# Kernel optimization log

Measured on AMD Instinct MI355X. Metric: run time of the kernel, lower is better.

The kernel has to match this reference:

```python
import jax, jax.numpy as jnp
import numpy as np

B, H, S, D = 1, 32, 2048, 128
LAST_Q = 64      # MInference uses the last 64 queries to estimate the pattern
V_TOPK = 256     # top vertical columns kept per head
S_TOPK = 512     # top slash diagonals kept per head
N_SINK = 4       # vertical columns always kept (attention sink)
N_LOCAL = 64     # local diagonals always kept
SCALE = 1.0 / np.sqrt(D)


def setup_inputs() -> dict:
    key = jax.random.key(0)
    k1, k2, k3 = jax.random.split(key, 3)
    q = jax.random.normal(k1, (B, H, S, D), jnp.float32)
    k = jax.random.normal(k2, (B, H, S, D), jnp.float32)
    v = jax.random.normal(k3, (B, H, S, D), jnp.float32)
    return {"q": q, "k": k, "v": v}


def _vertical_slash_masks(q, k):
    """Estimate per-head vertical/slash importance from the last LAST_Q queries
    and return boolean column mask [B,H,S] and diagonal mask [B,H,S]."""
    ql = q[:, :, -LAST_Q:, :]                                   # [B,H,LQ,D]
    est = jnp.einsum('bhqd,bhkd->bhqk', ql, k) * SCALE          # [B,H,LQ,S]
    rows = jnp.arange(S - LAST_Q, S)                            # global row ids
    cols = jnp.arange(S)
    causal = rows[:, None] >= cols[None, :]                     # [LQ,S]
    est = jnp.where(causal, est, -jnp.inf)
    p = jax.nn.softmax(est, axis=-1)                            # [B,H,LQ,S]

    # vertical importance: column sums of estimated attention
    vertical = p.sum(axis=2)                                    # [B,H,S]

    # slash importance: sums along diagonals d = row - col (d in [0, S-1])
    diag = jnp.clip(rows[:, None] - cols[None, :], 0, S - 1)    # negatives are causally masked (p=0)
    flat_d = diag.reshape(-1)
    flat_p = p.reshape(B * H, LAST_Q * S)
    slash = jax.vmap(lambda pr: jax.ops.segment_sum(pr, flat_d, num_segments=S))(flat_p)
    slash = slash.reshape(B, H, S)                              # [B,H,S]

    # always keep sink columns and the local diagonal band
    vertical = vertical.at[..., :N_SINK].set(jnp.inf)
    slash = slash.at[..., :N_LOCAL].set(jnp.inf)

    _, v_idx = jax.lax.top_k(vertical, V_TOPK)                  # [B,H,V_TOPK]
    _, s_idx = jax.lax.top_k(slash, S_TOPK)                     # [B,H,S_TOPK]

    scatter_true = jax.vmap(jax.vmap(lambda m, i: m.at[i].set(True)))
    vmask = scatter_true(jnp.zeros((B, H, S), bool), v_idx)     # which columns kept
    smask = scatter_true(jnp.zeros((B, H, S), bool), s_idx)     # which diagonals kept
    return vmask, smask


def reference(q, k, v):
    vmask, smask = _vertical_slash_masks(q, k)

    rows = jnp.arange(S)
    cols = jnp.arange(S)
    causal = rows[:, None] >= cols[None, :]                     # [S,S]
    d = jnp.clip(rows[:, None] - cols[None, :], 0, S - 1)       # [S,S] diagonal id

    # keep (r,c) if causal AND (column c is a top vertical OR diagonal r-c is a top slash)
    keep = causal[None, None] & (vmask[:, :, None, :] | jnp.take(smask, d, axis=-1))

    scores = jnp.einsum('bhqd,bhkd->bhqk', q, k) * SCALE        # [B,H,S,S]
    scores = jnp.where(keep, scores, -jnp.inf)
    probs = jax.nn.softmax(scores, axis=-1)                     # every row keeps diagonal 0 -> no all-masked rows
    return jnp.einsum('bhqk,bhkd->bhqd', probs, v)
```

## Files before the change

### kernel.cpp

```cpp
#include <hip/hip_runtime.h>
#include <hip/hip_bf16.h>

#define S_LEN 2048
#define NH 32
#define D_DIM 128
#define LAST_Q 64
#define SCALE_F 0.08838834764831845f
#define QSCALE (0.08838834764831845f * 1.4426950408889634f)
#define RESCALE_THR 11.54f

typedef __attribute__((ext_vector_type(8))) short bf16x8;
typedef __attribute__((ext_vector_type(4))) float f32x4;
typedef unsigned long long u64;
typedef unsigned int u32;
typedef unsigned short u16;

static __device__ __forceinline__ u16 f32_bf16(float f) {
  u32 u = __float_as_uint(f);
  u32 r = (u + 0x7FFFu + ((u >> 16) & 1u)) >> 16;
  return (u16)r;
}

static __device__ __forceinline__ u32 cvt_pk_bf16(float lo, float hi) {
  u32 r;
  asm("v_cvt_pk_bf16_f32 %0, %1, %2" : "=v"(r) : "v"(lo), "v"(hi));
  return r;
}

__global__ __launch_bounds__(256) void conv_kernel(const float* __restrict__ k,
                                                   const float* __restrict__ v,
                                                   u16* __restrict__ kpre,
                                                   u16* __restrict__ vpre) {
  int bid = blockIdx.x;
  int t = bid & 31, h = bid >> 5;
  int tid = threadIdx.x;
  int c0 = t * 64;
  __shared__ u16 Vb[64][136];
  for (int i = tid; i < 512; i += 256) {
    int r = i >> 3, s = i & 7;
    const float* srcp = v + ((size_t)(h * S_LEN + c0 + r)) * D_DIM + s * 16;
    float4 f0 = *(const float4*)(srcp);
    float4 f1 = *(const float4*)(srcp + 4);
    float4 f2 = *(const float4*)(srcp + 8);
    float4 f3 = *(const float4*)(srcp + 12);
    bf16x8 t0, t1;
    t0[0] = (short)f32_bf16(f0.x); t0[1] = (short)f32_bf16(f0.y);
    t0[2] = (short)f32_bf16(f0.z); t0[3] = (short)f32_bf16(f0.w);
    t0[4] = (short)f32_bf16(f1.x); t0[5] = (short)f32_bf16(f1.y);
    t0[6] = (short)f32_bf16(f1.z); t0[7] = (short)f32_bf16(f1.w);
    t1[0] = (short)f32_bf16(f2.x); t1[1] = (short)f32_bf16(f2.y);
    t1[2] = (short)f32_bf16(f2.z); t1[3] = (short)f32_bf16(f2.w);
    t1[4] = (short)f32_bf16(f3.x); t1[5] = (short)f32_bf16(f3.y);
    t1[6] = (short)f32_bf16(f3.z); t1[7] = (short)f32_bf16(f3.w);
    *(bf16x8*)&Vb[r][s * 16] = t0;
    *(bf16x8*)&Vb[r][s * 16 + 8] = t1;
  }
  u16* kp = kpre + (size_t)h * 262144 + (size_t)t * 8192;
#pragma unroll
  for (int j = 0; j < 4; ++j) {
    int p = j * 256 + tid;
    int r = p >> 4;
    int g = (p & 15) ^ (r & 15);
    const float* srcp = k + ((size_t)(h * S_LEN + c0 + r)) * D_DIM + g * 8;
    float4 a = *(const float4*)srcp;
    float4 b = *(const float4*)(srcp + 4);
    bf16x8 o;
    o[0] = (short)f32_bf16(a.x); o[1] = (short)f32_bf16(a.y);
    o[2] = (short)f32_bf16(a.z); o[3] = (short)f32_bf16(a.w);
    o[4] = (short)f32_bf16(b.x); o[5] = (short)f32_bf16(b.y);
    o[6] = (short)f32_bf16(b.z); o[7] = (short)f32_bf16(b.w);
    *(bf16x8*)(kp + p * 8) = o;
  }
  __syncthreads();
  u16* vp = vpre + (size_t)h * 262144 + (size_t)t * 8192;
#pragma unroll
  for (int j = 0; j < 4; ++j) {
    int p = j * 256 + tid;
    int d = p >> 3;
    int cb = (p & 7) ^ (d & 7);
    bf16x8 g;
#pragma unroll
    for (int e = 0; e < 8; ++e) g[e] = (short)Vb[cb * 8 + e][d];
    *(bf16x8*)(vp + p * 8) = g;
  }
}

__global__ __launch_bounds__(256) void est_kernel(const float* __restrict__ q,
                                                  const float* __restrict__ k,
                                                  float* __restrict__ scores) {
  int cc = blockIdx.x;
  int h = blockIdx.y;
  int tid = threadIdx.x;
  int ty = tid >> 4, tx = tid & 15;
  __shared__ float Qs[64][36];
  __shared__ float Ks[64][36];
  float acc[4][4];
#pragma unroll
  for (int i = 0; i < 4; ++i)
#pragma unroll
    for (int j = 0; j < 4; ++j) acc[i][j] = 0.f;
  const float* qbase = q + ((size_t)h * S_LEN + (S_LEN - LAST_Q)) * D_DIM;
  const float* kbase = k + ((size_t)h * S_LEN + cc * 64) * D_DIM;
  for (int dc = 0; dc < 4; ++dc) {
    __syncthreads();
    for (int i = tid; i < 512; i += 256) {
      int r = i >> 3, s = i & 7;
      float4 a = *(const float4*)(qbase + (size_t)r * D_DIM + dc * 32 + s * 4);
      *(float4*)&Qs[r][s * 4] = a;
      float4 b = *(const float4*)(kbase + (size_t)r * D_DIM + dc * 32 + s * 4);
      *(float4*)&Ks[r][s * 4] = b;
    }
    __syncthreads();
#pragma unroll
    for (int d4 = 0; d4 < 8; ++d4) {
      float4 qv[4], kv[4];
#pragma unroll
      for (int i = 0; i < 4; ++i) qv[i] = *(const float4*)&Qs[ty + 16 * i][d4 * 4];
#pragma unroll
      for (int j = 0; j < 4; ++j) kv[j] = *(const float4*)&Ks[tx + 16 * j][d4 * 4];
#pragma unroll
      for (int i = 0; i < 4; ++i)
#pragma unroll
        for (int j = 0; j < 4; ++j)
          acc[i][j] += qv[i].x * kv[j].x + qv[i].y * kv[j].y + qv[i].z * kv[j].z + qv[i].w * kv[j].w;
    }
  }
#pragma unroll
  for (int i = 0; i < 4; ++i) {
    int rl = ty + 16 * i;
    int rg = (S_LEN - LAST_Q) + rl;
#pragma unroll
    for (int j = 0; j < 4; ++j) {
      int cg = cc * 64 + tx + 16 * j;
      float vv = (cg <= rg) ? acc[i][j] * SCALE_F : -1e30f;
      scores[((size_t)h * LAST_Q + rl) * S_LEN + cg] = vv;
    }
  }
}

__global__ __launch_bounds__(256) void soft_partial_kernel(const float* __restrict__ scores,
                                                           float* __restrict__ part) {
  int h = blockIdx.x, rg = blockIdx.y;
  int tid = threadIdx.x;
  int wave = tid >> 6, lane = tid & 63;
  __shared__ float vs[2048];
  __shared__ float ss[2048];
  __shared__ float red[4];
  int i0 = tid * 8;
#pragma unroll
  for (int e = 0; e < 8; ++e) { vs[i0 + e] = 0.f; ss[i0 + e] = 0.f; }
  for (int rr = 0; rr < 8; ++rr) {
    int r = rg * 8 + rr;
    const float* sp = scores + ((size_t)h * LAST_Q + r) * S_LEN;
    float4 a = *(const float4*)(sp + i0);
    float4 b = *(const float4*)(sp + i0 + 4);
    float x[8] = {a.x, a.y, a.z, a.w, b.x, b.y, b.z, b.w};
    float wm = -1e30f;
#pragma unroll
    for (int e = 0; e < 8; ++e) wm = fmaxf(wm, x[e]);
#pragma unroll
    for (int mk = 1; mk < 64; mk <<= 1) wm = fmaxf(wm, __shfl_xor(wm, mk, 64));
    __syncthreads();
    if (lane == 0) red[wave] = wm;
    __syncthreads();
    float m = fmaxf(fmaxf(red[0], red[1]), fmaxf(red[2], red[3]));
    float psum = 0.f;
#pragma unroll
    for (int e = 0; e < 8; ++e) { x[e] = __expf(x[e] - m); psum += x[e]; }
#pragma unroll
    for (int mk = 1; mk < 64; mk <<= 1) psum += __shfl_xor(psum, mk, 64);
    __syncthreads();
    if (lane == 0) red[wave] = psum;
    __syncthreads();
    float inv = 1.f / (red[0] + red[1] + red[2] + red[3]);
    int rgl = (S_LEN - LAST_Q) + r;
#pragma unroll
    for (int e = 0; e < 8; ++e) {
      float p = x[e] * inv;
      int i = i0 + e;
      vs[i] += p;
      int d = rgl - i;
      if (d >= 0) ss[d] += p;
    }
  }
  __syncthreads();
  float* pb = part + ((size_t)(h * 8 + rg)) * 4096;
#pragma unroll
  for (int e = 0; e < 8; ++e) { pb[i0 + e] = vs[i0 + e]; pb[2048 + i0 + e] = ss[i0 + e]; }
}

__global__ __launch_bounds__(256) void topk_kernel(const float* __restrict__ part,
                                                   u64* __restrict__ vbits,
                                                   u64* __restrict__ sbits) {
  int h = blockIdx.x;
  int which = blockIdx.y;
  u64* dst = which ? (sbits + h * 32) : (vbits + h * 32);
  u32 K = which ? 512u : 256u;
  int ninf = which ? 64 : 4;
  int tid = threadIdx.x;
  int lane = tid & 63, wid = tid >> 6;
  __shared__ u32 keys[2048];
  __shared__ u32 hist[256];
  __shared__ u32 wpart[4];
  __shared__ u32 sh_pref, sh_kth;
  __shared__ u64 mbw[32];
  int i0 = tid * 8;
  float accv[8] = {0.f, 0.f, 0.f, 0.f, 0.f, 0.f, 0.f, 0.f};
  for (int rg = 0; rg < 8; ++rg) {
    const float* pp = part + ((size_t)(h * 8 + rg)) * 4096 + which * 2048 + i0;
    float4 a = *(const float4*)pp;
    float4 b = *(const float4*)(pp + 4);
    accv[0] += a.x; accv[1] += a.y; accv[2] += a.z; accv[3] += a.w;
    accv[4] += b.x; accv[5] += b.y; accv[6] += b.z; accv[7] += b.w;
  }
#pragma unroll
  for (int e = 0; e < 8; ++e) {
    int i = i0 + e;
    keys[i] = (i < ninf) ? 0x7F800000u : __float_as_uint(accv[e]);
  }
  __syncthreads();
  u32 prefix = 0;
  u32 kth = K;
  for (int shift = 24; shift >= 0; shift -= 8) {
    hist[tid] = 0;
    __syncthreads();
#pragma unroll
    for (int e = 0; e < 8; ++e) {
      u32 kk = keys[i0 + e];
      if (shift == 24 || (kk >> (shift + 8)) == (prefix >> (shift + 8)))
        atomicAdd(&hist[(kk >> shift) & 255], 1u);
    }
    __syncthreads();
    u32 v = hist[tid];
    u32 x = v;
#pragma unroll
    for (int off = 1; off < 64; off <<= 1) {
      u32 o = __shfl_up(x, off, 64);
      if (lane >= off) x += o;
    }
    if (lane == 63) wpart[wid] = x;
    __syncthreads();
    u32 base = 0;
    for (int w2 = 0; w2 < wid; ++w2) base += wpart[w2];
    u32 T = wpart[0] + wpart[1] + wpart[2] + wpart[3];
    u32 Pincl = x + base;
    u32 Sb = T - Pincl + v;
    u32 Sn = T - Pincl;
    if (Sb >= kth && Sn < kth) {
      sh_pref = prefix | ((u32)tid << shift);
      sh_kth = kth - Sn;
    }
    __syncthreads();
    prefix = sh_pref;
    kth = sh_kth;
    __syncthreads();
  }
  u32 t = prefix;
  u32 cnt = 0;
#pragma unroll
  for (int e = 0; e < 8; ++e) cnt += (keys[i0 + e] == t) ? 1u : 0u;
  u32 x = cnt;
#pragma unroll
  for (int off = 1; off < 64; off <<= 1) {
    u32 o = __shfl_up(x, off, 64);
    if (lane >= off) x += o;
  }
  if (lane == 63) wpart[wid] = x;
  __syncthreads();
  u32 base = 0;
  for (int w2 = 0; w2 < wid; ++w2) base += wpart[w2];
  u32 exc = x + base - cnt;
  unsigned char myb = 0;
  u32 seen = 0;
#pragma unroll
  for (int e = 0; e < 8; ++e) {
    u32 kk = keys[i0 + e];
    bool in = (kk > t) || (kk == t && (exc + seen) < kth);
    if (kk == t) ++seen;
    myb |= (in ? 1u : 0u) << e;
  }
  ((unsigned char*)mbw)[tid] = myb;
  __syncthreads();
  if (tid < 32) dst[tid] = mbw[tid];
}

template <bool PRE>
__global__ __launch_bounds__(256, 4) void attn_kernel(const float* __restrict__ q,
                                                      const float* __restrict__ kk,
                                                      const float* __restrict__ vv,
                                                      const u16* __restrict__ kpre,
                                                      const u16* __restrict__ vpre,
                                                      const u64* __restrict__ vbits,
                                                      const u64* __restrict__ sbits,
                                                      float* __restrict__ out) {
  int bid = blockIdx.x;
  int u = bid & 255, s = bid >> 8;
  int h = ((u >> 5) << 2) + s;
  int v_ = u & 31;
  int qt;
  switch (s) {
    case 0: qt = v_; break;
    case 1: qt = 31 - v_; break;
    case 2: qt = (v_ + 16) & 31; break;
    default: qt = (15 - v_) & 31; break;
  }
  int tid = threadIdx.x;
  int wave = tid >> 6, lane = tid & 63;
  int grp = lane >> 4, ln = lane & 15;

  __shared__ u16 Ks[8192];
  __shared__ u16 Vt[8192];
  __shared__ u64 smp[34];

  if (tid < 34) smp[tid] = (tid == 0 || tid == 33) ? 0ull : sbits[h * 32 + tid - 1];

  int q0w = qt * 64 + wave * 16;
  bf16x8 qf[4];
  const float* qrow = q + ((size_t)h * S_LEN + q0w + ln) * D_DIM;
#pragma unroll
  for (int ks = 0; ks < 4; ++ks) {
    const float* p = qrow + ks * 32 + grp * 8;
    float4 a = *(const float4*)p;
    float4 b = *(const float4*)(p + 4);
    bf16x8 f;
    f[0] = (short)f32_bf16(a.x * QSCALE); f[1] = (short)f32_bf16(a.y * QSCALE);
    f[2] = (short)f32_bf16(a.z * QSCALE); f[3] = (short)f32_bf16(a.w * QSCALE);
    f[4] = (short)f32_bf16(b.x * QSCALE); f[5] = (short)f32_bf16(b.y * QSCALE);
    f[6] = (short)f32_bf16(b.z * QSCALE); f[7] = (short)f32_bf16(b.w * QSCALE);
    qf[ks] = f;
  }
  f32x4 of[8];
#pragma unroll
  for (int i = 0; i < 8; ++i) of[i] = (f32x4){0.f, 0.f, 0.f, 0.f};
  float mr = -1e30f;
  float ls = 0.f;

  const u16* kp = kpre + (size_t)h * 262144;
  const u16* vp = vpre + (size_t)h * 262144;
  const float* kfb = kk + (size_t)h * S_LEN * D_DIM;
  const float* vfb = vv + (size_t)h * S_LEN * D_DIM;
  const u64* vwp = vbits + h * 32;
  int nt = qt + 1;
  int sb_lane = (lane & 48) + ((lane & 48) >> 2);

  auto issue_tile = [&](int t) {
    const u16* ksrc = kp + (size_t)t * 8192;
    const u16* vsrc = vp + (size_t)t * 8192;
#pragma unroll
    for (int i = 0; i < 4; ++i) {
      int chunk = wave * 4 + i;
      __builtin_amdgcn_global_load_lds(
          (const __attribute__((address_space(1))) u32*)(const void*)(ksrc + (size_t)(chunk * 64 + lane) * 8),
          (__attribute__((address_space(3))) u32*)(void*)(&Ks[chunk * 512]), 16, 0, 0);
      __builtin_amdgcn_global_load_lds(
          (const __attribute__((address_space(1))) u32*)(const void*)(vsrc + (size_t)(chunk * 64 + lane) * 8),
          (__attribute__((address_space(3))) u32*)(void*)(&Vt[chunk * 512]), 16, 0, 0);
    }
  };

  if constexpr (PRE) {
    issue_tile(0);
    asm volatile("s_waitcnt vmcnt(0)" ::: "memory");
  }
  __syncthreads();

  for (int t = 0; t < nt; ++t) {
    int c0 = t * 64;
    if constexpr (!PRE) {
      for (int i = tid; i < 512; i += 256) {
        int r = i >> 3, s2 = i & 7;
        const float* srcp = kfb + (size_t)(c0 + r) * D_DIM + s2 * 16;
        float4 f0 = *(const float4*)(srcp);
        float4 f1 = *(const float4*)(srcp + 4);
        float4 f2 = *(const float4*)(srcp + 8);
        float4 f3 = *(const float4*)(srcp + 12);
        bf16x8 t0, t1;
        t0[0] = (short)f32_bf16(f0.x); t0[1] = (short)f32_bf16(f0.y);
        t0[2] = (short)f32_bf16(f0.z); t0[3] = (short)f32_bf16(f0.w);
        t0[4] = (short)f32_bf16(f1.x); t0[5] = (short)f32_bf16(f1.y);
        t0[6] = (short)f32_bf16(f1.z); t0[7] = (short)f32_bf16(f1.w);
        t1[0] = (short)f32_bf16(f2.x); t1[1] = (short)f32_bf16(f2.y);
        t1[2] = (short)f32_bf16(f2.z); t1[3] = (short)f32_bf16(f2.w);
        t1[4] = (short)f32_bf16(f3.x); t1[5] = (short)f32_bf16(f3.y);
        t1[6] = (short)f32_bf16(f3.z); t1[7] = (short)f32_bf16(f3.w);
        int cb0 = s2 * 2, cb1 = s2 * 2 + 1;
        *(bf16x8*)&Ks[r * 128 + ((cb0 ^ (r & 15)) << 3)] = t0;
        *(bf16x8*)&Ks[r * 128 + ((cb1 ^ (r & 15)) << 3)] = t1;
      }
      for (int i = tid; i < 512; i += 256) {
        int r = i >> 3, s2 = i & 7;
        const float* srcp = vfb + (size_t)(c0 + r) * D_DIM + s2 * 16;
#pragma unroll
        for (int x = 0; x < 16; x += 4) {
          float4 f4 = *(const float4*)(srcp + x);
          int d0 = s2 * 16 + x;
          float vals[4] = {f4.x, f4.y, f4.z, f4.w};
#pragma unroll
          for (int y = 0; y < 4; ++y) {
            int d = d0 + y;
            Vt[d * 64 + (((r >> 3) ^ (d & 7)) << 3) + (r & 7)] = f32_bf16(vals[y]);
          }
        }
      }
      __syncthreads();
    }

    f32x4 sfr[4];
#pragma unroll
    for (int nb = 0; nb < 4; ++nb) {
      f32x4 acc = (f32x4){0.f, 0.f, 0.f, 0.f};
#pragma unroll
      for (int ks = 0; ks < 4; ++ks) {
        bf16x8 kf = *(const bf16x8*)&Ks[(nb * 16 + ln) * 128 + (((ks * 4 + grp) ^ ln) << 3)];
        acc = __builtin_amdgcn_mfma_f32_16x16x32_bf16(kf, qf[ks], acc, 0, 0, 0);
      }
      sfr[nb] = acc;
    }

    float tm = sfr[0][0];
#pragma unroll
    for (int nb = 0; nb < 4; ++nb)
#pragma unroll
      for (int jj = 0; jj < 4; ++jj) tm = fmaxf(tm, sfr[nb][jj]);
    tm = fmaxf(tm, __shfl_xor(tm, 16, 64));
    tm = fmaxf(tm, __shfl_xor(tm, 32, 64));

    if (__any(tm - mr > RESCALE_THR)) {
      float mn = fmaxf(mr, tm);
      float ex = exp2f(mr - mn);
      mr = mn;
      ls *= ex;
      float e0 = __shfl(ex, sb_lane, 64);
      float e1 = __shfl(ex, sb_lane + 1, 64);
      float e2 = __shfl(ex, sb_lane + 2, 64);
      float e3 = __shfl(ex, sb_lane + 3, 64);
#pragma unroll
      for (int db = 0; db < 8; ++db) {
        of[db][0] *= e0; of[db][1] *= e1; of[db][2] *= e2; of[db][3] *= e3;
      }
    }

    int Cb = (q0w + ln) - c0 - (grp << 2);
    float rs = 0.f;
    u32 pkw[8];
    if (c0 >= q0w - 48) {
#pragma unroll
      for (int nb = 0; nb < 4; ++nb) {
        float pv[4];
#pragma unroll
        for (int jj = 0; jj < 4; ++jj) {
          bool keep = (16 * nb + jj) <= Cb;
          float p = keep ? exp2f(sfr[nb][jj] - mr) : 0.f;
          rs += p;
          pv[jj] = p;
        }
        pkw[nb * 2] = cvt_pk_bf16(pv[0], pv[1]);
        pkw[nb * 2 + 1] = cvt_pk_bf16(pv[2], pv[3]);
      }
    } else {
      int b0 = Cb - 63;
      int w0i = (b0 >> 6) + 1;
      int sh = b0 & 63;
      u64 lo = smp[w0i];
      u64 hi = smp[w0i + 1];
      u64 W = (sh == 0) ? lo : ((lo >> sh) | (hi << (64 - sh)));
      u64 vword = vwp[t];
#pragma unroll
      for (int nb = 0; nb < 4; ++nb) {
        u32 vn = (u32)(vword >> (16 * nb + 4 * grp)) & 0xFu;
        u32 sn = (u32)(W >> (60 - 16 * nb)) & 0xFu;
        float pv[4];
#pragma unroll
        for (int jj = 0; jj < 4; ++jj) {
          u32 keep = ((vn >> jj) | (sn >> (3 - jj))) & 1u;
          float p = keep ? exp2f(sfr[nb][jj] - mr) : 0.f;
          rs += p;
          pv[jj] = p;
        }
        pkw[nb * 2] = cvt_pk_bf16(pv[0], pv[1]);
        pkw[nb * 2 + 1] = cvt_pk_bf16(pv[2], pv[3]);
      }
    }
    rs += __shfl_xor(rs, 16, 64);
    rs += __shfl_xor(rs, 32, 64);
    ls += rs;

#pragma unroll
    for (int ks2 = 0; ks2 < 2; ++ks2) {
      int sl0 = ln + ((lane & 16) << 1);
      int sl1 = sl0 + 16;
      u32 a0 = __shfl(pkw[ks2 * 4 + 0], sl0, 64);
      u32 a1 = __shfl(pkw[ks2 * 4 + 1], sl0, 64);
      u32 a2 = __shfl(pkw[ks2 * 4 + 0], sl1, 64);
      u32 a3 = __shfl(pkw[ks2 * 4 + 1], sl1, 64);
      u32 b0_ = __shfl(pkw[ks2 * 4 + 2], sl0, 64);
      u32 b1_ = __shfl(pkw[ks2 * 4 + 3], sl0, 64);
      u32 b2_ = __shfl(pkw[ks2 * 4 + 2], sl1, 64);
      u32 b3_ = __shfl(pkw[ks2 * 4 + 3], sl1, 64);
      bool hi2 = grp >= 2;
      union { u32 w[4]; bf16x8 v; } pu;
      pu.w[0] = hi2 ? b0_ : a0;
      pu.w[1] = hi2 ? b1_ : a1;
      pu.w[2] = hi2 ? b2_ : a2;
      pu.w[3] = hi2 ? b3_ : a3;
#pragma unroll
      for (int db = 0; db < 8; ++db) {
        int d = db * 16 + ln;
        bf16x8 vf = *(const bf16x8*)&Vt[d * 64 + ((((ks2 << 2) | grp) ^ (ln & 7)) << 3)];
        of[db] = __builtin_amdgcn_mfma_f32_16x16x32_bf16(pu.v, vf, of[db], 0, 0, 0);
      }
    }

    if (t + 1 < nt) {
      if constexpr (PRE) {
        __builtin_amdgcn_s_barrier();
        issue_tile(t + 1);
        asm volatile("s_waitcnt vmcnt(0)" ::: "memory");
        __builtin_amdgcn_s_barrier();
      } else {
        __syncthreads();
      }
    }
  }

  float invl = 1.f / ls;
  float i0 = __shfl(invl, sb_lane, 64);
  float i1 = __shfl(invl, sb_lane + 1, 64);
  float i2 = __shfl(invl, sb_lane + 2, 64);
  float i3 = __shfl(invl, sb_lane + 3, 64);
  float* ob = out + ((size_t)h * S_LEN + q0w) * D_DIM;
#pragma unroll
  for (int db = 0; db < 8; ++db) {
    ob[(size_t)(grp * 4 + 0) * D_DIM + db * 16 + ln] = of[db][0] * i0;
    ob[(size_t)(grp * 4 + 1) * D_DIM + db * 16 + ln] = of[db][1] * i1;
    ob[(size_t)(grp * 4 + 2) * D_DIM + db * 16 + ln] = of[db][2] * i2;
    ob[(size_t)(grp * 4 + 3) * D_DIM + db * 16 + ln] = of[db][3] * i3;
  }
}

extern "C" void kernel_launch(void* const* d_in, const int* in_sizes, int n_in,
                              void* d_out, int out_size, void* d_ws, size_t ws_size,
                              hipStream_t stream) {
  const float* q = (const float*)d_in[0];
  const float* k = (const float*)d_in[1];
  const float* v = (const float*)d_in[2];
  float* out = (float*)d_out;
  float* scores = out;
  float* part = out + 4194304;
  u64* vbits = (u64*)d_ws;
  u64* sbits = vbits + 1024;
  const size_t PRE_NEED = 16384 + 2ull * 16777216;
  bool pre = ws_size >= PRE_NEED;
  u16* kpre = (u16*)((char*)d_ws + 16384);
  u16* vpre = kpre + 8388608;

  if (pre) conv_kernel<<<1024, 256, 0, stream>>>(k, v, kpre, vpre);
  est_kernel<<<dim3(32, 32), 256, 0, stream>>>(q, k, scores);
  soft_partial_kernel<<<dim3(32, 8), 256, 0, stream>>>(scores, part);
  topk_kernel<<<dim3(32, 2), 256, 0, stream>>>(part, vbits, sbits);
  if (pre)
    attn_kernel<true><<<1024, 256, 0, stream>>>(q, k, v, kpre, vpre, vbits, sbits, out);
  else
    attn_kernel<false><<<1024, 256, 0, stream>>>(q, k, v, kpre, vpre, vbits, sbits, out);
}
```

Measured before the change: 161.7 us.

## Split K/V tile DMA to overlap next K load with PV compute

Splits the per-tile global-to-LDS load into separate K and V transfers. The next K tile is issued after the QK/softmax phase, so it overlaps the PV MFMAs, and the V tile is issued after PV with a partial vmcnt wait. The change also remaps block index to head/q-tile so consecutive blocks cover different heads, precomputes swizzled LDS offsets, and uses the raw hardware exp2 intrinsic. It adds extra barriers, and the vmcnt bookkeeping has to stay correct.

```diff
diff --git a/kernel.cpp b/kernel.cpp
--- a/kernel.cpp
+++ b/kernel.cpp
@@ -295,14 +295,14 @@
                                                       float* __restrict__ out) {
   int bid = blockIdx.x;
   int u = bid & 255, s = bid >> 8;
-  int h = ((u >> 5) << 2) + s;
-  int v_ = u & 31;
+  int h = u & 31;
+  int v_ = u >> 5;
   int qt;
   switch (s) {
     case 0: qt = v_; break;
     case 1: qt = 31 - v_; break;
-    case 2: qt = (v_ + 16) & 31; break;
-    default: qt = (15 - v_) & 31; break;
+    case 2: qt = v_ + 16; break;
+    default: qt = 15 - v_; break;
   }
   int tid = threadIdx.x;
   int wave = tid >> 6, lane = tid & 63;
@@ -335,6 +335,13 @@
   float mr = -1e30f;
   float ls = 0.f;
 
+  const int kb0 = (ln << 7) + (((0 + grp) ^ ln) << 3);
+  const int kb1 = (ln << 7) + (((4 + grp) ^ ln) << 3);
+  const int kb2 = (ln << 7) + (((8 + grp) ^ ln) << 3);
+  const int kb3 = (ln << 7) + (((12 + grp) ^ ln) << 3);
+  const int vb0 = (ln << 6) + (((0 + grp) ^ (ln & 7)) << 3);
+  const int vb1 = (ln << 6) + (((4 + grp) ^ (ln & 7)) << 3);
+
   const u16* kp = kpre + (size_t)h * 262144;
   const u16* vp = vpre + (size_t)h * 262144;
   const float* kfb = kk + (size_t)h * S_LEN * D_DIM;
@@ -343,25 +350,28 @@
   int nt = qt + 1;
   int sb_lane = (lane & 48) + ((lane & 48) >> 2);
 
-  auto issue_tile = [&](int t) {
+  auto dma_k = [&](int t) {
     const u16* ksrc = kp + (size_t)t * 8192;
-    const u16* vsrc = vp + (size_t)t * 8192;
 #pragma unroll
     for (int i = 0; i < 4; ++i) {
       int chunk = wave * 4 + i;
       __builtin_amdgcn_global_load_lds(
           (const __attribute__((address_space(1))) u32*)(const void*)(ksrc + (size_t)(chunk * 64 + lane) * 8),
           (__attribute__((address_space(3))) u32*)(void*)(&Ks[chunk * 512]), 16, 0, 0);
+    }
+  };
+  auto dma_v = [&](int t) {
+    const u16* vsrc = vp + (size_t)t * 8192;
+#pragma unroll
+    for (int i = 0; i < 4; ++i) {
+      int chunk = wave * 4 + i;
       __builtin_amdgcn_global_load_lds(
           (const __attribute__((address_space(1))) u32*)(const void*)(vsrc + (size_t)(chunk * 64 + lane) * 8),
           (__attribute__((address_space(3))) u32*)(void*)(&Vt[chunk * 512]), 16, 0, 0);
     }
   };
 
-  if constexpr (PRE) {
-    issue_tile(0);
-    asm volatile("s_waitcnt vmcnt(0)" ::: "memory");
-  }
+  if constexpr (PRE) { dma_k(0); dma_v(0); }
   __syncthreads();
 
   for (int t = 0; t < nt; ++t) {
@@ -409,11 +419,10 @@
 #pragma unroll
     for (int nb = 0; nb < 4; ++nb) {
       f32x4 acc = (f32x4){0.f, 0.f, 0.f, 0.f};
-#pragma unroll
-      for (int ks = 0; ks < 4; ++ks) {
-        bf16x8 kf = *(const bf16x8*)&Ks[(nb * 16 + ln) * 128 + (((ks * 4 + grp) ^ ln) << 3)];
-        acc = __builtin_amdgcn_mfma_f32_16x16x32_bf16(kf, qf[ks], acc, 0, 0, 0);
-      }
+      acc = __builtin_amdgcn_mfma_f32_16x16x32_bf16(*(const bf16x8*)&Ks[kb0 + nb * 2048], qf[0], acc, 0, 0, 0);
+      acc = __builtin_amdgcn_mfma_f32_16x16x32_bf16(*(const bf16x8*)&Ks[kb1 + nb * 2048], qf[1], acc, 0, 0, 0);
+      acc = __builtin_amdgcn_mfma_f32_16x16x32_bf16(*(const bf16x8*)&Ks[kb2 + nb * 2048], qf[2], acc, 0, 0, 0);
+      acc = __builtin_amdgcn_mfma_f32_16x16x32_bf16(*(const bf16x8*)&Ks[kb3 + nb * 2048], qf[3], acc, 0, 0, 0);
       sfr[nb] = acc;
     }
 
@@ -427,7 +436,7 @@
 
     if (__any(tm - mr > RESCALE_THR)) {
       float mn = fmaxf(mr, tm);
-      float ex = exp2f(mr - mn);
+      float ex = __builtin_amdgcn_exp2f(mr - mn);
       mr = mn;
       ls *= ex;
       float e0 = __shfl(ex, sb_lane, 64);
@@ -450,7 +459,7 @@
 #pragma unroll
         for (int jj = 0; jj < 4; ++jj) {
           bool keep = (16 * nb + jj) <= Cb;
-          float p = keep ? exp2f(sfr[nb][jj] - mr) : 0.f;
+          float p = keep ? __builtin_amdgcn_exp2f(sfr[nb][jj] - mr) : 0.f;
           rs += p;
           pv[jj] = p;
         }
@@ -473,7 +482,7 @@
 #pragma unroll
         for (int jj = 0; jj < 4; ++jj) {
           u32 keep = ((vn >> jj) | (sn >> (3 - jj))) & 1u;
-          float p = keep ? exp2f(sfr[nb][jj] - mr) : 0.f;
+          float p = keep ? __builtin_amdgcn_exp2f(sfr[nb][jj] - mr) : 0.f;
           rs += p;
           pv[jj] = p;
         }
@@ -484,6 +493,13 @@
     rs += __shfl_xor(rs, 16, 64);
     rs += __shfl_xor(rs, 32, 64);
     ls += rs;
+
+    if constexpr (PRE) {
+      __builtin_amdgcn_sched_barrier(0);
+      asm volatile("s_waitcnt vmcnt(0)" ::: "memory");
+      __builtin_amdgcn_s_barrier();
+      if (t + 1 < nt) dma_k(t + 1);
+    }
 
 #pragma unroll
     for (int ks2 = 0; ks2 < 2; ++ks2) {
@@ -503,23 +519,24 @@
       pu.w[1] = hi2 ? b1_ : a1;
       pu.w[2] = hi2 ? b2_ : a2;
       pu.w[3] = hi2 ? b3_ : a3;
+      int vb = ks2 ? vb1 : vb0;
 #pragma unroll
       for (int db = 0; db < 8; ++db) {
-        int d = db * 16 + ln;
-        bf16x8 vf = *(const bf16x8*)&Vt[d * 64 + ((((ks2 << 2) | grp) ^ (ln & 7)) << 3)];
+        bf16x8 vf = *(const bf16x8*)&Vt[vb + db * 1024];
         of[db] = __builtin_amdgcn_mfma_f32_16x16x32_bf16(pu.v, vf, of[db], 0, 0, 0);
       }
     }
 
-    if (t + 1 < nt) {
-      if constexpr (PRE) {
-        __builtin_amdgcn_s_barrier();
-        issue_tile(t + 1);
-        asm volatile("s_waitcnt vmcnt(0)" ::: "memory");
-        __builtin_amdgcn_s_barrier();
-      } else {
-        __syncthreads();
-      }
+    if constexpr (PRE) {
+      __builtin_amdgcn_sched_barrier(0);
+      __builtin_amdgcn_s_barrier();
+      if (t + 1 < nt) {
+        dma_v(t + 1);
+        asm volatile("s_waitcnt vmcnt(4)" ::: "memory");
+      }
+      __builtin_amdgcn_s_barrier();
+    } else {
+      __syncthreads();
     }
   }
 
```

New measurement: 140.9 us. -12.9%, faster.
